# Performance work log

Measured on AMD Instinct MI355X. Metric: run time of the kernel, lower is better.

## Reference

```python
import jax, jax.numpy as jnp
import numpy as np
import math

B = 16
D = 1024
K = 64
ALPHA = 0.0
N_MAX = 8192


def setup_inputs() -> dict:
    key = jax.random.key(0)
    k1, k2 = jax.random.split(key)
    lengths = jax.random.randint(k1, (B,), N_MAX // 2, N_MAX + 1)
    lengths = lengths.at[0].set(N_MAX)  # ensure max(lengths) == N_MAX, matching torch N_max
    lengths = lengths.astype(jnp.int64) if jax.config.jax_enable_x64 else lengths.astype(jnp.int32)
    W = jax.random.normal(k2, (D, 2 * K), dtype=jnp.float32) * (1.0 / math.sqrt(2 * K))
    return {"lengths": lengths, "W": W, "N_max": N_MAX}


def reference(lengths, W, N_max):
    # lengths: [B] int, W: [d, 2K] (torch Linear weight), N_max: python int
    d, twoK = W.shape
    Kk = twoK // 2
    k = jnp.arange(1, Kk + 1, dtype=jnp.float32)                      # [K]
    Delta = 2.0 * math.pi * k[None, :] / lengths[:, None].astype(jnp.float32)  # [B, K]
    t = jnp.arange(N_max, dtype=jnp.float32)                          # [N]
    theta = t[None, :, None] * Delta[:, None, :]                      # [B, N, K] closed-form angle
    amp = (k ** (-ALPHA)) * (1.0 / math.sqrt(Kk))                     # [K]
    # interleave (cos, sin) pairs along last dim: [c1,s1,c2,s2,...]
    cs = jnp.stack([jnp.cos(theta), jnp.sin(theta)], axis=-1)         # [B, N, K, 2]
    feats = (cs * amp[None, None, :, None]).reshape(theta.shape[0], N_max, twoK)
    mask = jnp.arange(N_max)[None, :] < lengths[:, None]              # [B, N]
    feats = feats * mask[:, :, None].astype(feats.dtype)
    pos_emb = jnp.einsum('bnf,df->bnd', feats, W)                     # [B, N, d]
    return pos_emb, mask
```

## Files before the change

kernel.cpp:

```cpp
#include <hip/hip_runtime.h>
#include <math.h>

#define B_DIM    16
#define D_DIM    1024
#define K_FREQ   64
#define F_DIM    128
#define N_MAXLEN 8192

#define BM   128
#define BN   128
#define LDSS 136

typedef __attribute__((ext_vector_type(8))) short bf16x8;
typedef __attribute__((ext_vector_type(4))) float f32x4;

__device__ __forceinline__ unsigned short f2bf(float x) {
    union { float f; unsigned u; } v; v.f = x;
    unsigned r = (v.u + 0x7FFFu + ((v.u >> 16) & 1u)) >> 16;
    return (unsigned short)r;
}

__global__ __launch_bounds__(256, 2) void cyclic_gemm_kernel(
    const int* __restrict__ lengths,
    const float* __restrict__ W,
    float* __restrict__ out)
{
    __shared__ short sA[BM * LDSS];
    __shared__ short sB[BN * LDSS];

    const int tid = threadIdx.x;
    const int m0  = blockIdx.y * BM;
    const int d0  = blockIdx.x * BN;

    {
        const int r    = tid >> 1;
        const int half = tid & 1;
        const int m    = m0 + r;
        const int b    = m >> 13;
        const int n    = m & (N_MAXLEN - 1);
        const int len  = lengths[b];
        unsigned* dst = (unsigned*)&sA[r * LDSS + half * 64];
        if (n >= len) {
            #pragma unroll
            for (int j = 0; j < 32; ++j) dst[j] = 0u;
        } else {
            const float base = (float)n / (float)len;
            #pragma unroll
            for (int j = 0; j < 32; ++j) {
                const int k = half * 32 + j;
                float rev = base * (float)(k + 1);
                rev -= floorf(rev);
                float s, c;
                __sincosf(6.283185307179586f * rev, &s, &c);
                const unsigned cb = f2bf(c * 0.125f);
                const unsigned sb = f2bf(s * 0.125f);
                dst[j] = cb | (sb << 16);
            }
        }
    }

    {
        const float4* Wv = (const float4*)(W + (size_t)d0 * F_DIM);
        #pragma unroll
        for (int i = 0; i < 16; ++i) {
            const int lin = tid + i * 256;
            const int row = lin >> 5;
            const int c4  = lin & 31;
            const float4 w = Wv[row * 32 + c4];
            unsigned* p = (unsigned*)&sB[row * LDSS + c4 * 4];
            p[0] = (unsigned)f2bf(w.x) | ((unsigned)f2bf(w.y) << 16);
            p[1] = (unsigned)f2bf(w.z) | ((unsigned)f2bf(w.w) << 16);
        }
    }

    __syncthreads();

    const int lane = tid & 63;
    const int wave = tid >> 6;
    const int wm   = (wave >> 1) * 64;
    const int wn   = (wave & 1) * 64;
    const int lrow = lane & 15;
    const int quad = lane >> 4;

    f32x4 acc[4][4];
    #pragma unroll
    for (int mi = 0; mi < 4; ++mi)
        #pragma unroll
        for (int ni = 0; ni < 4; ++ni)
            acc[mi][ni] = (f32x4){0.f, 0.f, 0.f, 0.f};

    const short* aBase = &sA[(wm + lrow) * LDSS + quad * 8];
    const short* bBase = &sB[(wn + lrow) * LDSS + quad * 8];

    #pragma unroll
    for (int ks = 0; ks < 4; ++ks) {
        bf16x8 af[4], bfr[4];
        #pragma unroll
        for (int i = 0; i < 4; ++i) {
            af[i]  = *(const bf16x8*)(aBase + i * 16 * LDSS + ks * 32);
            bfr[i] = *(const bf16x8*)(bBase + i * 16 * LDSS + ks * 32);
        }
        #pragma unroll
        for (int mi = 0; mi < 4; ++mi)
            #pragma unroll
            for (int ni = 0; ni < 4; ++ni)
                acc[mi][ni] = __builtin_amdgcn_mfma_f32_16x16x32_bf16(
                    af[mi], bfr[ni], acc[mi][ni], 0, 0, 0);
    }

    #pragma unroll
    for (int mi = 0; mi < 4; ++mi) {
        #pragma unroll
        for (int reg = 0; reg < 4; ++reg) {
            const int row = m0 + wm + mi * 16 + quad * 4 + reg;
            float* orow = out + (size_t)row * D_DIM + (d0 + wn + lrow);
            #pragma unroll
            for (int ni = 0; ni < 4; ++ni)
                orow[ni * 16] = acc[mi][ni][reg];
        }
    }
}

__global__ void mask_kernel(const int* __restrict__ lengths, float* __restrict__ maskp) {
    const int i = blockIdx.x * blockDim.x + threadIdx.x;
    const int b = i >> 13;
    const int n = i & (N_MAXLEN - 1);
    maskp[i] = (n < lengths[b]) ? 1.0f : 0.0f;
}

extern "C" void kernel_launch(void* const* d_in, const int* in_sizes, int n_in,
                              void* d_out, int out_size, void* d_ws, size_t ws_size,
                              hipStream_t stream) {
    const int*   lengths = (const int*)d_in[0];
    const float* W       = (const float*)d_in[1];
    float* out   = (float*)d_out;
    float* maskp = out + (size_t)B_DIM * N_MAXLEN * D_DIM;

    dim3 grid(D_DIM / BN, (B_DIM * N_MAXLEN) / BM);
    cyclic_gemm_kernel<<<grid, dim3(256), 0, stream>>>(lengths, W, out);

    const int mtot = B_DIM * N_MAXLEN;
    mask_kernel<<<mtot / 256, dim3(256), 0, stream>>>(lengths, maskp);
}
```

Measured before the change: 519.4 us.

## Generate A fragments in registers, shrink N tile, stage output through LDS for vector stores

The sin/cos feature fragments are now computed directly into MFMA register layout with hardware sin/cos intrinsics, so the LDS staging of A is gone. The 0.125 amplitude moves into W. BN is halved so each block uses less LDS and can run at higher occupancy (launch bounds 4). Accumulators are transposed through LDS so each thread writes full 16-byte rows, replacing scattered scalar stores. The cost is redundant trig work across the column blocks and extra barriers in the epilogue.

```diff
diff --git a/kernel.cpp b/kernel.cpp
--- a/kernel.cpp
+++ b/kernel.cpp
@@ -1,122 +1,128 @@
 #include <hip/hip_runtime.h>
+#include <hip/hip_bf16.h>
 #include <math.h>
 
 #define B_DIM    16
 #define D_DIM    1024
-#define K_FREQ   64
 #define F_DIM    128
 #define N_MAXLEN 8192
 
 #define BM   128
-#define BN   128
-#define LDSS 136
+#define BN   64
+#define SBS  136
+#define STS  68
 
 typedef __attribute__((ext_vector_type(8))) short bf16x8;
 typedef __attribute__((ext_vector_type(4))) float f32x4;
 
-__device__ __forceinline__ unsigned short f2bf(float x) {
-    union { float f; unsigned u; } v; v.f = x;
-    unsigned r = (v.u + 0x7FFFu + ((v.u >> 16) & 1u)) >> 16;
-    return (unsigned short)r;
-}
+union BF2 { __hip_bfloat162 h; unsigned u; };
+union FRAG { unsigned u[4]; bf16x8 v; };
 
-__global__ __launch_bounds__(256, 2) void cyclic_gemm_kernel(
+__global__ __launch_bounds__(256, 4) void cyclic_gemm_kernel(
     const int* __restrict__ lengths,
     const float* __restrict__ W,
     float* __restrict__ out)
 {
-    __shared__ short sA[BM * LDSS];
-    __shared__ short sB[BN * LDSS];
+    __shared__ __align__(16) char smem[BN * SBS * 2];
+    short* sB = (short*)smem;
+    float* sT = (float*)smem;
 
     const int tid = threadIdx.x;
     const int m0  = blockIdx.y * BM;
     const int d0  = blockIdx.x * BN;
-
-    {
-        const int r    = tid >> 1;
-        const int half = tid & 1;
-        const int m    = m0 + r;
-        const int b    = m >> 13;
-        const int n    = m & (N_MAXLEN - 1);
-        const int len  = lengths[b];
-        unsigned* dst = (unsigned*)&sA[r * LDSS + half * 64];
-        if (n >= len) {
-            #pragma unroll
-            for (int j = 0; j < 32; ++j) dst[j] = 0u;
-        } else {
-            const float base = (float)n / (float)len;
-            #pragma unroll
-            for (int j = 0; j < 32; ++j) {
-                const int k = half * 32 + j;
-                float rev = base * (float)(k + 1);
-                rev -= floorf(rev);
-                float s, c;
-                __sincosf(6.283185307179586f * rev, &s, &c);
-                const unsigned cb = f2bf(c * 0.125f);
-                const unsigned sb = f2bf(s * 0.125f);
-                dst[j] = cb | (sb << 16);
-            }
-        }
-    }
+    const int b   = m0 >> 13;
+    const int n0  = m0 & (N_MAXLEN - 1);
+    const int len = lengths[b];
 
     {
         const float4* Wv = (const float4*)(W + (size_t)d0 * F_DIM);
         #pragma unroll
-        for (int i = 0; i < 16; ++i) {
+        for (int i = 0; i < 8; ++i) {
             const int lin = tid + i * 256;
             const int row = lin >> 5;
             const int c4  = lin & 31;
-            const float4 w = Wv[row * 32 + c4];
-            unsigned* p = (unsigned*)&sB[row * LDSS + c4 * 4];
-            p[0] = (unsigned)f2bf(w.x) | ((unsigned)f2bf(w.y) << 16);
-            p[1] = (unsigned)f2bf(w.z) | ((unsigned)f2bf(w.w) << 16);
+            const float4 w = Wv[lin];
+            BF2 p0, p1;
+            p0.h = __float22bfloat162_rn(make_float2(w.x * 0.125f, w.y * 0.125f));
+            p1.h = __float22bfloat162_rn(make_float2(w.z * 0.125f, w.w * 0.125f));
+            unsigned* p = (unsigned*)&sB[row * SBS + c4 * 4];
+            p[0] = p0.u; p[1] = p1.u;
         }
     }
 
-    __syncthreads();
-
     const int lane = tid & 63;
     const int wave = tid >> 6;
-    const int wm   = (wave >> 1) * 64;
-    const int wn   = (wave & 1) * 64;
     const int lrow = lane & 15;
     const int quad = lane >> 4;
 
-    f32x4 acc[4][4];
+    bf16x8 af[2][4];
     #pragma unroll
-    for (int mi = 0; mi < 4; ++mi)
+    for (int mi = 0; mi < 2; ++mi) {
+        const int n     = n0 + wave * 32 + mi * 16 + lrow;
+        const bool valid = n < len;
+        const float base = (float)n / (float)len;
+        #pragma unroll
+        for (int ks = 0; ks < 4; ++ks) {
+            FRAG f;
+            #pragma unroll
+            for (int p = 0; p < 4; ++p) {
+                const float kf1 = (float)(ks * 16 + quad * 4 + p + 1);
+                float rev = base * kf1;
+                rev -= floorf(rev);
+                const float c = __builtin_amdgcn_cosf(rev);
+                const float s = __builtin_amdgcn_sinf(rev);
+                BF2 cs; cs.h = __float22bfloat162_rn(make_float2(c, s));
+                f.u[p] = valid ? cs.u : 0u;
+            }
+            af[mi][ks] = f.v;
+        }
+    }
+
+    f32x4 acc[2][4];
+    #pragma unroll
+    for (int mi = 0; mi < 2; ++mi)
         #pragma unroll
         for (int ni = 0; ni < 4; ++ni)
             acc[mi][ni] = (f32x4){0.f, 0.f, 0.f, 0.f};
 
-    const short* aBase = &sA[(wm + lrow) * LDSS + quad * 8];
-    const short* bBase = &sB[(wn + lrow) * LDSS + quad * 8];
+    __syncthreads();
 
     #pragma unroll
     for (int ks = 0; ks < 4; ++ks) {
-        bf16x8 af[4], bfr[4];
+        bf16x8 bf[4];
         #pragma unroll
-        for (int i = 0; i < 4; ++i) {
-            af[i]  = *(const bf16x8*)(aBase + i * 16 * LDSS + ks * 32);
-            bfr[i] = *(const bf16x8*)(bBase + i * 16 * LDSS + ks * 32);
-        }
+        for (int ni = 0; ni < 4; ++ni)
+            bf[ni] = *(const bf16x8*)&sB[(ni * 16 + lrow) * SBS + ks * 32 + quad * 8];
         #pragma unroll
-        for (int mi = 0; mi < 4; ++mi)
+        for (int mi = 0; mi < 2; ++mi)
             #pragma unroll
             for (int ni = 0; ni < 4; ++ni)
                 acc[mi][ni] = __builtin_amdgcn_mfma_f32_16x16x32_bf16(
-                    af[mi], bfr[ni], acc[mi][ni], 0, 0, 0);
+                    af[mi][ks], bf[ni], acc[mi][ni], 0, 0, 0);
     }
 
     #pragma unroll
-    for (int mi = 0; mi < 4; ++mi) {
+    for (int h = 0; h < 2; ++h) {
+        __syncthreads();
+        if ((wave >> 1) == h) {
+            const int rbase = (wave & 1) * 32;
+            #pragma unroll
+            for (int mi = 0; mi < 2; ++mi)
+                #pragma unroll
+                for (int ni = 0; ni < 4; ++ni)
+                    #pragma unroll
+                    for (int reg = 0; reg < 4; ++reg)
+                        sT[(rbase + mi * 16 + quad * 4 + reg) * STS + lrow + ni * 16]
+                            = acc[mi][ni][reg];
+        }
+        __syncthreads();
         #pragma unroll
-        for (int reg = 0; reg < 4; ++reg) {
-            const int row = m0 + wm + mi * 16 + quad * 4 + reg;
-            float* orow = out + (size_t)row * D_DIM + (d0 + wn + lrow);
-            #pragma unroll
-            for (int ni = 0; ni < 4; ++ni)
-                orow[ni * 16] = acc[mi][ni][reg];
+        for (int i = 0; i < 4; ++i) {
+            const int idx = tid + i * 256;
+            const int row = idx >> 4;
+            const int c4  = idx & 15;
+            const f32x4 v = *(const f32x4*)&sT[row * STS + c4 * 4];
+            *(f32x4*)&out[(size_t)(m0 + h * 64 + row) * D_DIM + d0 + c4 * 4] = v;
         }
     }
 }
```

Measured after the change: 520.4 us. About the same (+0.2%).
